# Kernel tuning notes

Hardware: AMD Instinct MI355X
Metric: run time of the kernel (lower is better)

Reference implementation:

```python
import jax, jax.numpy as jnp
import numpy as np

V = 32          # number_variables
DEG = 12        # degree
ORDER = 3       # spline_order (cubic)
N_BASIS = DEG + ORDER - 1  # 14, rows of params
LO, HI = -15.0, 15.0       # polynomial_range[:, 0]
EPS = 1e-6


def make_knots():
    dist = (HI - LO) / (DEG - 1)
    k = DEG + 2 * ORDER
    return jnp.linspace(LO - ORDER * dist, HI + ORDER * dist, k, dtype=jnp.float32)


def bspline_basis(x, knots, order):
    # x: [N, P] -> basis: [N, P, N_BASIS] via Cox-de Boor recursion (Naive_Basis)
    xk = x[..., None]
    b = ((xk >= knots[:-1]) & (xk < knots[1:])).astype(x.dtype)  # degree-0, [N,P,K-1]
    t = knots
    for k in range(1, order + 1):
        left = (xk - t[:-(k + 1)]) / (t[k:-1] - t[:-(k + 1)])
        right = (t[k + 1:] - xk) / (t[k + 1:] - t[1:-k])
        b = left * b[..., :-1] + right * b[..., 1:]
    return b  # [N, P, K-1-order] == [N, P, N_BASIS]


def setup_inputs() -> dict:
    key = jax.random.key(0)
    k1, k2 = jax.random.split(key)
    num_lambdas = V * (V - 1) // 2  # 496
    inp = jax.random.normal(k1, (16384, V), dtype=jnp.float32)
    log_d = jnp.zeros((16384, V), dtype=jnp.float32)
    params = 0.001 * jnp.ones((N_BASIS, num_lambdas), dtype=jnp.float32)
    return {"input": inp, "log_d": log_d, "params": params}


def reference(input, log_d, params):
    n = input.shape[0]
    knots = make_knots()
    rows, cols = np.tril_indices(V, -1)  # matches torch.tril_indices(V, V, offset=-1)
    rows = jnp.asarray(rows); cols = jnp.asarray(cols)
    # clamp into half-open spline support for valid degree-0 basis
    x = jnp.clip(input, LO, HI - EPS)
    xs = x[:, cols]                                  # [N, P] per-pair covariate values
    basis = bspline_basis(xs, knots, ORDER)          # [N, P, N_BASIS]
    lam = jnp.einsum('npk,kp->np', basis, params)    # [N, P] lambda values
    # lower-triangular lambda matrix: identity + strict lower entries
    lm = jnp.broadcast_to(jnp.eye(V, dtype=input.dtype), (n, V, V))
    lm = lm.at[:, rows, cols].set(lam)
    out = jnp.einsum('nvc,nc->nv', lm, input)        # bmm(lambda_matrix, input)
    # ridge penalties on spline coefficients (penalize_towards=0)
    d2 = jnp.diff(params, n=2, axis=0)
    d1 = jnp.diff(params, n=1, axis=0)
    second_pen = jnp.sum(d2 ** 2)
    first_pen = jnp.sum(d1 ** 2)
    param_pen = jnp.sum(params ** 2)
    return out, lm, second_pen, first_pen, param_pen
```

## Files before the change

### kernel.cpp

```cpp
#include <hip/hip_runtime.h>

#define VDIM   32
#define NPAIR  496
#define NBASIS 14
#define NPARAM (NBASIS * NPAIR)
#define NINT   11
#define ROWS   8
#define LROW   544

typedef float f32x4 __attribute__((ext_vector_type(4)));

__device__ __forceinline__ int seg_of(int v) {
    int m = v - 1;
    if (m <= 0) return 0;
    int q = m >> 2, r = m & 3;
    return 4 * (2 * q * (q + 1) + r * (q + 1));
}

__global__ __launch_bounds__(256) void Decorrelation_prep(
    const float* __restrict__ params,
    f32x4* __restrict__ ptv,
    float* __restrict__ pens)
{
    const int tid = threadIdx.x;
    const int i   = blockIdx.x;
    for (int p = tid; p < NPAIR; p += 256) {
        f32x4 w = { params[(i    ) * NPAIR + p],
                    params[(i + 1) * NPAIR + p],
                    params[(i + 2) * NPAIR + p],
                    params[(i + 3) * NPAIR + p] };
        ptv[i * NPAIR + p] = w;
    }
    if (blockIdx.x == 0) {
        float s2 = 0.f, s1 = 0.f, sp = 0.f;
        for (int idx = tid; idx < NPARAM; idx += 256) {
            const float a = params[idx];
            sp += a * a;
            if (idx < NPARAM - NPAIR) {
                const float b = params[idx + NPAIR];
                const float d1 = b - a;
                s1 += d1 * d1;
                if (idx < NPARAM - 2 * NPAIR) {
                    const float c = params[idx + 2 * NPAIR];
                    const float d2 = c - 2.f * b + a;
                    s2 += d2 * d2;
                }
            }
        }
        #pragma unroll
        for (int off = 32; off > 0; off >>= 1) {
            s2 += __shfl_down(s2, off);
            s1 += __shfl_down(s1, off);
            sp += __shfl_down(sp, off);
        }
        __shared__ float ws[3][4];
        const int lane = tid & 63, wid = tid >> 6;
        if (lane == 0) { ws[0][wid] = s2; ws[1][wid] = s1; ws[2][wid] = sp; }
        __syncthreads();
        if (tid == 0) {
            pens[0] = ws[0][0] + ws[0][1] + ws[0][2] + ws[0][3];
            pens[1] = ws[1][0] + ws[1][1] + ws[1][2] + ws[1][3];
            pens[2] = ws[2][0] + ws[2][1] + ws[2][2] + ws[2][3];
        }
    }
}

__global__ __launch_bounds__(256) void Decorrelation_35270271435435_kernel(
    const float* __restrict__ input,
    const f32x4* __restrict__ ptv,
    float* __restrict__ out,
    float* __restrict__ lm,
    int N)
{
    __shared__ f32x4         wgt4[ROWS][VDIM];
    __shared__ float         xin [ROWS][VDIM];
    __shared__ unsigned char ibk [ROWS][VDIM];
    __shared__ float         lam [ROWS][LROW];

    const int tid = threadIdx.x;
    const int n0  = blockIdx.x * ROWS;

    {
        const int r = tid >> 5, c = tid & 31;
        const int n = n0 + r;
        const float xi = (n < N) ? input[n * VDIM + c] : 0.0f;
        xin[r][c] = xi;
        const float dist = 30.0f / 11.0f;
        const float invd = 11.0f / 30.0f;
        const float t0   = -15.0f - 3.0f * dist;
        float x = fminf(fmaxf(xi, -15.0f), 15.0f - 1e-6f);
        float u = (x - t0) * invd;
        int   i = (int)floorf(u);
        i = min(13, max(3, i));
        const float uu  = u - (float)i;
        const float om  = 1.0f - uu;
        const float uu2 = uu * uu, uu3 = uu2 * uu;
        const float sixth = 1.0f / 6.0f;
        f32x4 w = { om * om * om * sixth,
                    (3.0f * uu3 - 6.0f * uu2 + 4.0f) * sixth,
                    (-3.0f * uu3 + 3.0f * uu2 + 3.0f * uu + 1.0f) * sixth,
                    uu3 * sixth };
        wgt4[r][c] = w;
        ibk[r][c]  = (unsigned char)(i - 3);
    }

    const int p1 = tid;
    int v1 = (int)((1.0f + sqrtf(8.0f * (float)p1 + 1.0f)) * 0.5f);
    while (v1 * (v1 - 1) / 2 > p1) --v1;
    while ((v1 + 1) * v1 / 2 <= p1) ++v1;
    const int c1 = p1 - v1 * (v1 - 1) / 2;
    const int o1 = seg_of(v1) + c1;

    const int  p2   = tid + 256;
    const bool has2 = (p2 < NPAIR);
    int c2 = 0, o2 = 0;
    if (has2) {
        int v2 = (int)((1.0f + sqrtf(8.0f * (float)p2 + 1.0f)) * 0.5f);
        while (v2 * (v2 - 1) / 2 > p2) --v2;
        while ((v2 + 1) * v2 / 2 <= p2) ++v2;
        c2 = p2 - v2 * (v2 - 1) / 2;
        o2 = seg_of(v2) + c2;
    }
    __syncthreads();

    #pragma unroll
    for (int r = 0; r < ROWS; ++r) {
        {
            const int   i = ibk[r][c1];
            const f32x4 w = wgt4[r][c1];
            const f32x4 q = ptv[i * NPAIR + p1];
            lam[r][o1] = w.x * q.x + w.y * q.y + w.z * q.z + w.w * q.w;
        }
        if (has2) {
            const int   i = ibk[r][c2];
            const f32x4 w = wgt4[r][c2];
            const f32x4 q = ptv[i * NPAIR + p2];
            lam[r][o2] = w.x * q.x + w.y * q.y + w.z * q.z + w.w * q.w;
        }
    }
    __syncthreads();

    const int v    = tid >> 3;
    const int c0   = (tid & 7) << 2;
    const int segv = seg_of(v);
    float* lmp = lm + (size_t)n0 * (VDIM * VDIM) + tid * 4;

    #pragma unroll
    for (int r = 0; r < ROWS; ++r, lmp += VDIM * VDIM) {
        const int n = n0 + r;
        if (n >= N) break;
        const f32x4 lq = *(const f32x4*)&lam[r][segv + c0];
        const f32x4 xq = *(const f32x4*)&xin[r][c0];
        float vals[4];
        float partial = 0.0f;
        #pragma unroll
        for (int j = 0; j < 4; ++j) {
            const int c = c0 + j;
            const float lv = (j == 0) ? lq.x : (j == 1) ? lq.y : (j == 2) ? lq.z : lq.w;
            const float xv = (j == 0) ? xq.x : (j == 1) ? xq.y : (j == 2) ? xq.z : xq.w;
            const float val = (c < v) ? lv : ((c == v) ? 1.0f : 0.0f);
            vals[j] = val;
            partial += val * xv;
        }
        f32x4 f4 = { vals[0], vals[1], vals[2], vals[3] };
        *(f32x4*)lmp = f4;

        partial += __shfl_down(partial, 4, 8);
        partial += __shfl_down(partial, 2, 8);
        partial += __shfl_down(partial, 1, 8);
        if ((tid & 7) == 0) out[n * VDIM + v] = partial;
    }
}

extern "C" void kernel_launch(void* const* d_in, const int* in_sizes, int n_in,
                              void* d_out, int out_size, void* d_ws, size_t ws_size,
                              hipStream_t stream) {
    const float* input  = (const float*)d_in[0];
    const float* params = (const float*)d_in[2];
    const int N = in_sizes[0] / VDIM;

    float* out  = (float*)d_out;
    float* lm   = out + (size_t)N * VDIM;
    float* pens = lm + (size_t)N * VDIM * VDIM;

    f32x4* ptv = (f32x4*)d_ws;

    Decorrelation_prep<<<NINT, 256, 0, stream>>>(params, ptv, pens);

    const int nb = (N + ROWS - 1) / ROWS;
    Decorrelation_35270271435435_kernel<<<nb, 256, 0, stream>>>(
        input, ptv, out, lm, N);
}
```

Baseline: 97.55 us.

## Compute spline weights per pair inline and stream lambda matrix with nontemporal stores

The main kernel drops the shared-memory staging of spline weights, knot indices and inputs. Each pair thread now reads its input value from global memory and evaluates the cubic weights itself, which removes one barrier but repeats the weight arithmetic once per pair instead of once per variable. The large lambda-matrix output is written with nontemporal stores, and the kernel gets a launch-bounds occupancy hint. The penalty reduction moves to its own extra block in the prep kernel so it no longer delays interval block 0, and the N bounds check is removed, which assumes N is a multiple of ROWS.

```diff
diff --git a/kernel.cpp b/kernel.cpp
--- a/kernel.cpp
+++ b/kernel.cpp
@@ -23,26 +23,28 @@
     float* __restrict__ pens)
 {
     const int tid = threadIdx.x;
-    const int i   = blockIdx.x;
-    for (int p = tid; p < NPAIR; p += 256) {
-        f32x4 w = { params[(i    ) * NPAIR + p],
-                    params[(i + 1) * NPAIR + p],
-                    params[(i + 2) * NPAIR + p],
-                    params[(i + 3) * NPAIR + p] };
-        ptv[i * NPAIR + p] = w;
-    }
-    if (blockIdx.x == 0) {
+    const int b   = blockIdx.x;
+    if (b < NINT) {
+        const int i = b;
+        for (int p = tid; p < NPAIR; p += 256) {
+            f32x4 w = { params[(i    ) * NPAIR + p],
+                        params[(i + 1) * NPAIR + p],
+                        params[(i + 2) * NPAIR + p],
+                        params[(i + 3) * NPAIR + p] };
+            ptv[i * NPAIR + p] = w;
+        }
+    } else {
         float s2 = 0.f, s1 = 0.f, sp = 0.f;
         for (int idx = tid; idx < NPARAM; idx += 256) {
             const float a = params[idx];
             sp += a * a;
             if (idx < NPARAM - NPAIR) {
-                const float b = params[idx + NPAIR];
-                const float d1 = b - a;
+                const float bb = params[idx + NPAIR];
+                const float d1 = bb - a;
                 s1 += d1 * d1;
                 if (idx < NPARAM - 2 * NPAIR) {
-                    const float c = params[idx + 2 * NPAIR];
-                    const float d2 = c - 2.f * b + a;
+                    const float cc = params[idx + 2 * NPAIR];
+                    const float d2 = cc - 2.f * bb + a;
                     s2 += d2 * d2;
                 }
             }
@@ -65,44 +67,17 @@
     }
 }
 
-__global__ __launch_bounds__(256) void Decorrelation_35270271435435_kernel(
+__global__ __launch_bounds__(256, 4) void Decorrelation_35270271435435_kernel(
     const float* __restrict__ input,
     const f32x4* __restrict__ ptv,
     float* __restrict__ out,
     float* __restrict__ lm,
     int N)
 {
-    __shared__ f32x4         wgt4[ROWS][VDIM];
-    __shared__ float         xin [ROWS][VDIM];
-    __shared__ unsigned char ibk [ROWS][VDIM];
-    __shared__ float         lam [ROWS][LROW];
+    __shared__ float lam[ROWS][LROW];
 
     const int tid = threadIdx.x;
     const int n0  = blockIdx.x * ROWS;
-
-    {
-        const int r = tid >> 5, c = tid & 31;
-        const int n = n0 + r;
-        const float xi = (n < N) ? input[n * VDIM + c] : 0.0f;
-        xin[r][c] = xi;
-        const float dist = 30.0f / 11.0f;
-        const float invd = 11.0f / 30.0f;
-        const float t0   = -15.0f - 3.0f * dist;
-        float x = fminf(fmaxf(xi, -15.0f), 15.0f - 1e-6f);
-        float u = (x - t0) * invd;
-        int   i = (int)floorf(u);
-        i = min(13, max(3, i));
-        const float uu  = u - (float)i;
-        const float om  = 1.0f - uu;
-        const float uu2 = uu * uu, uu3 = uu2 * uu;
-        const float sixth = 1.0f / 6.0f;
-        f32x4 w = { om * om * om * sixth,
-                    (3.0f * uu3 - 6.0f * uu2 + 4.0f) * sixth,
-                    (-3.0f * uu3 + 3.0f * uu2 + 3.0f * uu + 1.0f) * sixth,
-                    uu3 * sixth };
-        wgt4[r][c] = w;
-        ibk[r][c]  = (unsigned char)(i - 3);
-    }
 
     const int p1 = tid;
     int v1 = (int)((1.0f + sqrtf(8.0f * (float)p1 + 1.0f)) * 0.5f);
@@ -121,21 +96,46 @@
         c2 = p2 - v2 * (v2 - 1) / 2;
         o2 = seg_of(v2) + c2;
     }
-    __syncthreads();
 
-    #pragma unroll
+    const float dist  = 30.0f / 11.0f;
+    const float invd  = 11.0f / 30.0f;
+    const float t0    = -15.0f - 3.0f * dist;
+    const float sixth = 1.0f / 6.0f;
+
+    #pragma unroll 4
     for (int r = 0; r < ROWS; ++r) {
+        const int base = (n0 + r) * VDIM;
         {
-            const int   i = ibk[r][c1];
-            const f32x4 w = wgt4[r][c1];
-            const f32x4 q = ptv[i * NPAIR + p1];
-            lam[r][o1] = w.x * q.x + w.y * q.y + w.z * q.z + w.w * q.w;
+            const float xi = input[base + c1];
+            float x = fminf(fmaxf(xi, -15.0f), 15.0f - 1e-6f);
+            float u = (x - t0) * invd;
+            int   i = (int)floorf(u);
+            i = min(13, max(3, i));
+            const float uu  = u - (float)i;
+            const float om  = 1.0f - uu;
+            const float uu2 = uu * uu, uu3 = uu2 * uu;
+            const float w0 = om * om * om * sixth;
+            const float w1 = (3.0f * uu3 - 6.0f * uu2 + 4.0f) * sixth;
+            const float w2 = (-3.0f * uu3 + 3.0f * uu2 + 3.0f * uu + 1.0f) * sixth;
+            const float w3 = uu3 * sixth;
+            const f32x4 q  = ptv[(i - 3) * NPAIR + p1];
+            lam[r][o1] = w0 * q.x + w1 * q.y + w2 * q.z + w3 * q.w;
         }
         if (has2) {
-            const int   i = ibk[r][c2];
-            const f32x4 w = wgt4[r][c2];
-            const f32x4 q = ptv[i * NPAIR + p2];
-            lam[r][o2] = w.x * q.x + w.y * q.y + w.z * q.z + w.w * q.w;
+            const float xi = input[base + c2];
+            float x = fminf(fmaxf(xi, -15.0f), 15.0f - 1e-6f);
+            float u = (x - t0) * invd;
+            int   i = (int)floorf(u);
+            i = min(13, max(3, i));
+            const float uu  = u - (float)i;
+            const float om  = 1.0f - uu;
+            const float uu2 = uu * uu, uu3 = uu2 * uu;
+            const float w0 = om * om * om * sixth;
+            const float w1 = (3.0f * uu3 - 6.0f * uu2 + 4.0f) * sixth;
+            const float w2 = (-3.0f * uu3 + 3.0f * uu2 + 3.0f * uu + 1.0f) * sixth;
+            const float w3 = uu3 * sixth;
+            const f32x4 q  = ptv[(i - 3) * NPAIR + p2];
+            lam[r][o2] = w0 * q.x + w1 * q.y + w2 * q.z + w3 * q.w;
         }
     }
     __syncthreads();
@@ -148,9 +148,8 @@
     #pragma unroll
     for (int r = 0; r < ROWS; ++r, lmp += VDIM * VDIM) {
         const int n = n0 + r;
-        if (n >= N) break;
         const f32x4 lq = *(const f32x4*)&lam[r][segv + c0];
-        const f32x4 xq = *(const f32x4*)&xin[r][c0];
+        const f32x4 xq = *(const f32x4*)(input + n * VDIM + c0);
         float vals[4];
         float partial = 0.0f;
         #pragma unroll
@@ -163,7 +162,7 @@
             partial += val * xv;
         }
         f32x4 f4 = { vals[0], vals[1], vals[2], vals[3] };
-        *(f32x4*)lmp = f4;
+        __builtin_nontemporal_store(f4, (f32x4*)lmp);
 
         partial += __shfl_down(partial, 4, 8);
         partial += __shfl_down(partial, 2, 8);
@@ -185,7 +184,7 @@
 
     f32x4* ptv = (f32x4*)d_ws;
 
-    Decorrelation_prep<<<NINT, 256, 0, stream>>>(params, ptv, pens);
+    Decorrelation_prep<<<NINT + 1, 256, 0, stream>>>(params, ptv, pens);
 
     const int nb = (N + ROWS - 1) / ROWS;
     Decorrelation_35270271435435_kernel<<<nb, 256, 0, stream>>>(
```

Measured after the change: 103.2 us. 1.06x slower.
